# Kernel tuning notes

Hardware: AMD Instinct MI355X
Metric: run time of the kernel (lower is better)

Reference implementation:

```python
import jax, jax.numpy as jnp
import numpy as np

B, T, F, E = 256, 100, 34, 1024


def setup_inputs() -> dict:
    key = jax.random.key(0)
    ks = jax.random.split(key, 12)
    sc = 1.0 / np.sqrt(E)
    u = lambda k, shape: jax.random.uniform(k, shape, jnp.float32, -sc, sc)
    return {
        "x": jax.random.normal(ks[0], (B, T, F), jnp.float32),
        "W_lin": u(ks[1], (E, F)),
        "b_lin": u(ks[2], (E,)),
        "W_ih1": u(ks[3], (4 * E, E)),
        "W_hh1": u(ks[4], (4 * E, E)),
        "b_ih1": u(ks[5], (4 * E,)),
        "b_hh1": u(ks[6], (4 * E,)),
        "W_ih2": u(ks[7], (4 * E, E)),
        "W_hh2": u(ks[8], (4 * E, E)),
        "b_ih2": u(ks[9], (4 * E,)),
        "b_hh2": u(ks[10], (4 * E,)),
    }


def _gate_update(gates, c):
    # torch LSTMCell gate order: input, forget, cell(g), output
    i, f, g, o = jnp.split(gates, 4, axis=-1)
    c_new = jax.nn.sigmoid(f) * c + jax.nn.sigmoid(i) * jnp.tanh(g)
    h_new = jax.nn.sigmoid(o) * jnp.tanh(c_new)
    return h_new, c_new


def reference(x, W_lin, b_lin, W_ih1, W_hh1, b_ih1, b_hh1, W_ih2, W_hh2, b_ih2, b_hh2):
    hd = W_hh1.shape[1]
    bsz = x.shape[0]
    enc = x @ W_lin.T + b_lin                      # [B,T,E]
    # Precompute layer-1 input projections (incl. both biases) for all timesteps
    xg1 = jnp.einsum('bte,ge->btg', enc, W_ih1) + (b_ih1 + b_hh1)  # [B,T,4E]
    xs = jnp.swapaxes(xg1, 0, 1)                   # [T,B,4E] time-major for scan
    b2 = b_ih2 + b_hh2
    z = jnp.zeros((bsz, hd), jnp.float32)

    def step(carry, xg):
        h1, c1, h2, c2 = carry
        h1, c1 = _gate_update(xg + h1 @ W_hh1.T, c1)
        h2, c2 = _gate_update(h1 @ W_ih2.T + b2 + h2 @ W_hh2.T, c2)
        return (h1, c1, h2, c2), None

    (h1, c1, h2, c2), _ = jax.lax.scan(step, (z, z, z, z), xs)
    return (h2, c2)
```

## Files before the change

### kernel.cpp

```cpp
#include <hip/hip_runtime.h>

#define USH unsigned short
#define AGENT __HIP_MEMORY_SCOPE_AGENT
typedef __attribute__((ext_vector_type(8))) short short8;
typedef __attribute__((ext_vector_type(4))) float f32x4;

__device__ __forceinline__ USH rne_bf16(float f){
  unsigned int u = __float_as_uint(f);
  u = (u + 0x7fffu + ((u >> 16) & 1u)) >> 16;
  return (USH)u;
}
__device__ __forceinline__ float sigm(float x){ return 1.f / (1.f + __expf(-x)); }
__device__ __forceinline__ float tanh_(float x){ return 1.f - 2.f / (__expf(2.f * x) + 1.f); }
__device__ __forceinline__ void gload16(const void* g, void* l){
  __builtin_amdgcn_global_load_lds((const __attribute__((address_space(1))) unsigned int*)g,
                                   (__attribute__((address_space(3))) unsigned int*)l, 16, 0, 0);
}
__device__ __forceinline__ void st_bf16_sc1(USH* p, USH v){
  asm volatile("global_store_short %0, %1, off sc1" :: "v"(p), "v"((unsigned int)v) : "memory");
}
#define MFMA __builtin_amdgcn_mfma_f32_16x16x32_bf16

__global__ void k_fold(const float* __restrict__ Wih1, const float* __restrict__ Wlin,
                       const float* __restrict__ blin, const float* __restrict__ bih1,
                       const float* __restrict__ bhh1, USH* __restrict__ Wcpk, float* __restrict__ bc){
  const int n = blockIdx.x;
  const int t = threadIdx.x;
  float a[34];
#pragma unroll
  for (int f = 0; f < 34; ++f) a[f] = 0.f;
  float ab = 0.f;
  for (int e = t; e < 1024; e += 64){
    const float wv = Wih1[n * 1024 + e];
    ab += wv * blin[e];
    const float* wl = Wlin + e * 34;
#pragma unroll
    for (int f = 0; f < 34; ++f) a[f] += wv * wl[f];
  }
#pragma unroll
  for (int off = 32; off > 0; off >>= 1){
    ab += __shfl_down(ab, off);
#pragma unroll
    for (int f = 0; f < 34; ++f) a[f] += __shfl_down(a[f], off);
  }
  if (t == 0){
    const int nc = n & 1023, gq = n >> 10, cgi = nc >> 4, lp = nc & 15;
    for (int f = 0; f < 64; ++f){
      const float v = (f < 34) ? a[f] : 0.f;
      const int lane = lp + (((f >> 3) & 3) << 4);
      const int idx = (((cgi * 2 + (f >> 5)) * 4 + gq) * 64 + lane) * 8 + (f & 7);
      Wcpk[idx] = rne_bf16(v);
    }
    bc[n] = ab + bih1[n] + bhh1[n];
  }
}

__global__ void k_pack(const float* __restrict__ Whh1, const float* __restrict__ Wih2,
                       const float* __restrict__ Whh2, const float* __restrict__ bih2,
                       const float* __restrict__ bhh2,
                       USH* __restrict__ P1, USH* __restrict__ P2a, USH* __restrict__ P2b,
                       float* __restrict__ ob2){
  const int N = 4096 * 1024;
  for (int i = blockIdx.x * blockDim.x + threadIdx.x; i < N; i += gridDim.x * blockDim.x){
    const int j = i & 7, li = (i >> 3) & 63, gq = (i >> 9) & 3, ks = (i >> 11) & 31, cgi = i >> 16;
    const int n = gq * 1024 + cgi * 16 + (li & 15);
    const int k = ks * 32 + ((li >> 4) << 3) + j;
    const int src = n * 1024 + k;
    P1[i]  = rne_bf16(Whh1[src]);
    P2a[i] = rne_bf16(Wih2[src]);
    P2b[i] = rne_bf16(Whh2[src]);
    if (i < 4096) ob2[i] = bih2[i] + bhh2[i];
  }
}

__global__ void k_xpk(const float* __restrict__ x, USH* __restrict__ xp){
  const int N = 100 * 16384;
  for (int i = blockIdx.x * blockDim.x + threadIdx.x; i < N; i += gridDim.x * blockDim.x){
    const int j = i & 7, li = (i >> 3) & 63, ks = (i >> 9) & 1, g = (i >> 10) & 15, t = i >> 14;
    const int row = g * 16 + (li & 15);
    const int f = ks * 32 + ((li >> 4) << 3) + j;
    xp[i] = (f < 34) ? rne_bf16(x[(row * 100 + t) * 34 + f]) : (USH)0;
  }
}

__global__ __launch_bounds__(256) void k_persist(
    USH* __restrict__ hA1, USH* __restrict__ hA2,
    int* __restrict__ ctrA, int* __restrict__ ctrB,
    const USH* __restrict__ Wpk1, const USH* __restrict__ Wpk2a, const USH* __restrict__ Wpk2b,
    const USH* __restrict__ Wcpk, const USH* __restrict__ xpk,
    const float* __restrict__ bc, const float* __restrict__ b2, float* __restrict__ out,
    int d1, int d2, int useFence)
{
  __shared__ __attribute__((aligned(16))) char lds[131072];
  const int tid = threadIdx.x, w = tid >> 6, l = tid & 63;
  const int wg = blockIdx.x;
  const int isL2 = wg >> 7;
  const int cg = (wg & 127) >> 1;
  const int mh = wg & 1;
  const int gb = mh * 8 + w * 2;
  const int col = cg * 16 + (l & 15);
  const int lofs16 = l * 16;
  const int lofs8 = l * 8;

  if (!isL2){
    const USH* s = Wpk1 + (size_t)cg * 65536;
#pragma unroll
    for (int r = 0; r < 32; ++r)
      gload16(s + (r * 4 + w) * 512 + lofs8, &lds[(r * 4 + w) * 1024]);
  } else {
    const USH* s = Wpk2b + (size_t)cg * 65536;
#pragma unroll
    for (int r = 0; r < 24; ++r)
      gload16(s + (r * 4 + w) * 512 + lofs8, &lds[(r * 4 + w) * 1024]);
  }

  short8 wc[2][4];
  if (!isL2){
#pragma unroll
    for (int ks = 0; ks < 2; ++ks)
#pragma unroll
      for (int gq = 0; gq < 4; ++gq)
        wc[ks][gq] = *(const short8*)(Wcpk + (size_t)cg * 4096 + (ks * 4 + gq) * 512 + lofs8);
  }
  __syncthreads();

  float bi0, bi1, bi2, bi3;
  { const float* bs = isL2 ? b2 : bc;
    bi0 = bs[col]; bi1 = bs[1024 + col]; bi2 = bs[2048 + col]; bi3 = bs[3072 + col]; }

  float creg[2][4];
#pragma unroll
  for (int mf = 0; mf < 2; ++mf)
#pragma unroll
    for (int r = 0; r < 4; ++r) creg[mf][r] = 0.f;

  const int ks2 = cg >> 1;
  const int l16 = (cg * 2 + ((l & 15) >> 3)) & 3;
  const int j2 = l & 7;

  for (int p = 0; p <= 100; ++p){
    const bool active = isL2 ? (p >= 1) : (p < 100);
    if (active){
      f32x4 acc[2][4];
#pragma unroll
      for (int mf = 0; mf < 2; ++mf)
#pragma unroll
        for (int gq = 0; gq < 4; ++gq) acc[mf][gq] = (f32x4){0.f, 0.f, 0.f, 0.f};

      if (!isL2){
        if (p > 0){
          const USH* Ap = hA1 + (size_t)((p - 1) % d1) * 262144 + gb * 16384 + lofs8;
#pragma unroll
          for (int ks = 0; ks < 32; ++ks){
            short8 a0 = *(const short8*)(Ap + ks * 512);
            short8 a1 = *(const short8*)(Ap + 16384 + ks * 512);
            const char* bb = &lds[ks * 4096 + lofs16];
#pragma unroll
            for (int gq = 0; gq < 4; ++gq){
              short8 bf = *(const short8*)(bb + gq * 1024);
              acc[0][gq] = MFMA(a0, bf, acc[0][gq], 0, 0, 0);
              acc[1][gq] = MFMA(a1, bf, acc[1][gq], 0, 0, 0);
            }
          }
        }
        const USH* Xp = xpk + (size_t)p * 16384 + gb * 1024 + lofs8;
#pragma unroll
        for (int ks = 0; ks < 2; ++ks){
          short8 a0 = *(const short8*)(Xp + ks * 512);
          short8 a1 = *(const short8*)(Xp + 1024 + ks * 512);
#pragma unroll
          for (int gq = 0; gq < 4; ++gq){
            acc[0][gq] = MFMA(a0, wc[ks][gq], acc[0][gq], 0, 0, 0);
            acc[1][gq] = MFMA(a1, wc[ks][gq], acc[1][gq], 0, 0, 0);
          }
        }
        USH* hn = hA1 + (size_t)(p % d1) * 262144;
#pragma unroll
        for (int mf = 0; mf < 2; ++mf){
          const int g2 = gb + mf;
#pragma unroll
          for (int r = 0; r < 4; ++r){
            const float gi = acc[mf][0][r] + bi0;
            const float gf = acc[mf][1][r] + bi1;
            const float gg = acc[mf][2][r] + bi2;
            const float go = acc[mf][3][r] + bi3;
            const float cn = sigm(gf) * creg[mf][r] + sigm(gi) * tanh_(gg);
            creg[mf][r] = cn;
            const int lane2 = ((l >> 4) << 2) + r + (l16 << 4);
            st_bf16_sc1(&hn[(g2 * 32 + ks2) * 512 + lane2 * 8 + j2], rne_bf16(sigm(go) * tanh_(cn)));
          }
        }
      } else {
        const USH* A1p = hA1 + (size_t)((p - 1) % d1) * 262144 + gb * 16384 + lofs8;
        const USH* A2p = hA2 + (size_t)((p - 1) % d2) * 262144 + gb * 16384 + lofs8;
        const USH* Wsa = Wpk2a + (size_t)cg * 65536;
        const USH* Wsb = Wpk2b + (size_t)cg * 65536;
        short8 ar[2][8];
#pragma unroll
        for (int r = 0; r < 4; ++r)
          gload16(Wsa + (r * 4 + w) * 512 + lofs8, &lds[98304 + (r * 4 + w) * 1024]);
#pragma unroll
        for (int kk = 0; kk < 4; ++kk){
          ar[0][kk * 2]     = *(const short8*)(A1p + kk * 512);
          ar[0][kk * 2 + 1] = *(const short8*)(A1p + 16384 + kk * 512);
        }
#pragma unroll
        for (int c = 0; c < 10; ++c){
          __syncthreads();
          if (c < 9){
            const int t = c + 1;
            const USH* src = (t < 8) ? (Wsa + t * 8192) : (Wsb + (t - 2) * 8192);
            char* dst = &lds[98304 + (t & 1) * 16384];
#pragma unroll
            for (int r = 0; r < 4; ++r)
              gload16(src + (r * 4 + w) * 512 + lofs8, dst + (r * 4 + w) * 1024);
            const USH* Ab = (t < 8) ? A1p : A2p;
            const int ksb = (t < 8) ? t * 4 : (t - 2) * 4;
#pragma unroll
            for (int kk = 0; kk < 4; ++kk){
              ar[t & 1][kk * 2]     = *(const short8*)(Ab + (ksb + kk) * 512);
              ar[t & 1][kk * 2 + 1] = *(const short8*)(Ab + 16384 + (ksb + kk) * 512);
            }
          }
          const char* cb = &lds[98304 + (c & 1) * 16384 + lofs16];
#pragma unroll
          for (int kk = 0; kk < 4; ++kk){
#pragma unroll
            for (int gq = 0; gq < 4; ++gq){
              short8 bf = *(const short8*)(cb + kk * 4096 + gq * 1024);
              acc[0][gq] = MFMA(ar[c & 1][kk * 2],     bf, acc[0][gq], 0, 0, 0);
              acc[1][gq] = MFMA(ar[c & 1][kk * 2 + 1], bf, acc[1][gq], 0, 0, 0);
            }
          }
        }
#pragma unroll
        for (int ks = 0; ks < 24; ++ks){
          short8 a0 = *(const short8*)(A2p + ks * 512);
          short8 a1 = *(const short8*)(A2p + 16384 + ks * 512);
          const char* bb = &lds[ks * 4096 + lofs16];
#pragma unroll
          for (int gq = 0; gq < 4; ++gq){
            short8 bf = *(const short8*)(bb + gq * 1024);
            acc[0][gq] = MFMA(a0, bf, acc[0][gq], 0, 0, 0);
            acc[1][gq] = MFMA(a1, bf, acc[1][gq], 0, 0, 0);
          }
        }
        if (p < 100){
          USH* hn = hA2 + (size_t)(p % d2) * 262144;
#pragma unroll
          for (int mf = 0; mf < 2; ++mf){
            const int g2 = gb + mf;
#pragma unroll
            for (int r = 0; r < 4; ++r){
              const float gi = acc[mf][0][r] + bi0;
              const float gf = acc[mf][1][r] + bi1;
              const float gg = acc[mf][2][r] + bi2;
              const float go = acc[mf][3][r] + bi3;
              const float cn = sigm(gf) * creg[mf][r] + sigm(gi) * tanh_(gg);
              creg[mf][r] = cn;
              const int lane2 = ((l >> 4) << 2) + r + (l16 << 4);
              st_bf16_sc1(&hn[(g2 * 32 + ks2) * 512 + lane2 * 8 + j2], rne_bf16(sigm(go) * tanh_(cn)));
            }
          }
        } else {
#pragma unroll
          for (int mf = 0; mf < 2; ++mf){
#pragma unroll
            for (int r = 0; r < 4; ++r){
              const int row = (gb + mf) * 16 + ((l >> 4) << 2) + r;
              const float gi = acc[mf][0][r] + bi0;
              const float gf = acc[mf][1][r] + bi1;
              const float gg = acc[mf][2][r] + bi2;
              const float go = acc[mf][3][r] + bi3;
              const float cn = sigm(gf) * creg[mf][r] + sigm(gi) * tanh_(gg);
              out[row * 1024 + col] = sigm(go) * tanh_(cn);
              out[262144 + row * 1024 + col] = cn;
            }
          }
        }
      }
    }
    if (p < 100){
      asm volatile("s_waitcnt vmcnt(0)" ::: "memory");
      __syncthreads();
      if (tid == 0){
        if (useFence) __builtin_amdgcn_fence(__ATOMIC_RELEASE, "agent");
        __hip_atomic_fetch_add(isL2 ? ctrB : ctrA, 1, __ATOMIC_RELAXED, AGENT);
        const int q = p + 1;
        const int tA = 128 * q;
        const int tB = isL2 ? 128 * q : 128 * (q - 1);
        while (__hip_atomic_load(ctrA, __ATOMIC_RELAXED, AGENT) < tA)
          __builtin_amdgcn_s_sleep(1);
        while (__hip_atomic_load(ctrB, __ATOMIC_RELAXED, AGENT) < tB)
          __builtin_amdgcn_s_sleep(1);
        if (useFence) __builtin_amdgcn_fence(__ATOMIC_ACQUIRE, "agent");
      }
      __syncthreads();
    }
  }
}

extern "C" void kernel_launch(void* const* d_in, const int* in_sizes, int n_in,
                              void* d_out, int out_size, void* d_ws, size_t ws_size,
                              hipStream_t stream){
  const float* x    = (const float*)d_in[0];
  const float* Wlin = (const float*)d_in[1];
  const float* blin = (const float*)d_in[2];
  const float* Wih1 = (const float*)d_in[3];
  const float* Whh1 = (const float*)d_in[4];
  const float* bih1 = (const float*)d_in[5];
  const float* bhh1 = (const float*)d_in[6];
  const float* Wih2 = (const float*)d_in[7];
  const float* Whh2 = (const float*)d_in[8];
  const float* bih2 = (const float*)d_in[9];
  const float* bhh2 = (const float*)d_in[10];
  char* ws = (char*)d_ws;

  const size_t SLOT = 524288;
  int d1 = 100, d2 = 100, useFence = 0;
  const size_t need = 1024 + 200 * SLOT + 3 * 8388608ull + 524288 + 3276800 + 32768;
  if (ws_size < need){ d1 = 3; d2 = 2; useFence = 1; }

  size_t off = 0;
  int*   ctrA  = (int*)(ws + off);  off += 128;
  int*   ctrB  = (int*)(ws + off);  off = 1024;
  USH*   hA2   = (USH*)(ws + off);  off += (size_t)d2 * SLOT;
  USH*   hA1   = (USH*)(ws + off);  off += (size_t)d1 * SLOT;
  USH*   Wpk1  = (USH*)(ws + off);  off += 8388608;
  USH*   Wpk2a = (USH*)(ws + off);  off += 8388608;
  USH*   Wpk2b = (USH*)(ws + off);  off += 8388608;
  USH*   Wcpk  = (USH*)(ws + off);  off += 524288;
  USH*   xpk   = (USH*)(ws + off);  off += 3276800;
  float* bc    = (float*)(ws + off); off += 16384;
  float* b2    = (float*)(ws + off);

  hipMemsetAsync(ws, 0, 1024 + 2 * SLOT, stream);
  k_fold<<<4096, 64, 0, stream>>>(Wih1, Wlin, blin, bih1, bhh1, Wcpk, bc);
  k_pack<<<2048, 256, 0, stream>>>(Whh1, Wih2, Whh2, bih2, bhh2, Wpk1, Wpk2a, Wpk2b, b2);
  k_xpk<<<1024, 256, 0, stream>>>(x, xpk);

  float* outp = (float*)d_out;
  void* args[] = {&hA1, &hA2, &ctrA, &ctrB, &Wpk1, &Wpk2a, &Wpk2b, &Wcpk, &xpk, &bc, &b2, &outp,
                  &d1, &d2, &useFence};
  hipError_t e = hipLaunchCooperativeKernel((void*)k_persist, dim3(256), dim3(256), args, 0, stream);
  if (e != hipSuccess){
    k_persist<<<dim3(256), dim3(256), 0, stream>>>(hA1, hA2, ctrA, ctrB, Wpk1, Wpk2a, Wpk2b,
                                                   Wcpk, xpk, bc, b2, outp, d1, d2, useFence);
  }
}
```

Measured before the change: 1.760 ms.

## Split layer loops and relax grid barrier to per-layer dependency waits

```diff
diff --git a/kernel.cpp b/kernel.cpp
--- a/kernel.cpp
+++ b/kernel.cpp
@@ -102,79 +102,190 @@
   const int lofs16 = l * 16;
   const int lofs8 = l * 8;
 
-  if (!isL2){
-    const USH* s = Wpk1 + (size_t)cg * 65536;
-#pragma unroll
-    for (int r = 0; r < 32; ++r)
-      gload16(s + (r * 4 + w) * 512 + lofs8, &lds[(r * 4 + w) * 1024]);
-  } else {
-    const USH* s = Wpk2b + (size_t)cg * 65536;
-#pragma unroll
-    for (int r = 0; r < 24; ++r)
-      gload16(s + (r * 4 + w) * 512 + lofs8, &lds[(r * 4 + w) * 1024]);
-  }
-
-  short8 wc[2][4];
-  if (!isL2){
-#pragma unroll
-    for (int ks = 0; ks < 2; ++ks)
-#pragma unroll
-      for (int gq = 0; gq < 4; ++gq)
-        wc[ks][gq] = *(const short8*)(Wcpk + (size_t)cg * 4096 + (ks * 4 + gq) * 512 + lofs8);
-  }
-  __syncthreads();
-
-  float bi0, bi1, bi2, bi3;
-  { const float* bs = isL2 ? b2 : bc;
-    bi0 = bs[col]; bi1 = bs[1024 + col]; bi2 = bs[2048 + col]; bi3 = bs[3072 + col]; }
-
-  float creg[2][4];
-#pragma unroll
-  for (int mf = 0; mf < 2; ++mf)
-#pragma unroll
-    for (int r = 0; r < 4; ++r) creg[mf][r] = 0.f;
-
   const int ks2 = cg >> 1;
   const int l16 = (cg * 2 + ((l & 15) >> 3)) & 3;
   const int j2 = l & 7;
 
-  for (int p = 0; p <= 100; ++p){
-    const bool active = isL2 ? (p >= 1) : (p < 100);
-    if (active){
+  float creg[2][4];
+#pragma unroll
+  for (int mf = 0; mf < 2; ++mf)
+#pragma unroll
+    for (int r = 0; r < 4; ++r) creg[mf][r] = 0.f;
+
+  if (!isL2){
+    const USH* s = Wpk1 + (size_t)cg * 65536;
+#pragma unroll
+    for (int r = 0; r < 32; ++r)
+      gload16(s + (r * 4 + w) * 512 + lofs8, &lds[(r * 4 + w) * 1024]);
+    short8 wc[2][4];
+#pragma unroll
+    for (int ks = 0; ks < 2; ++ks)
+#pragma unroll
+      for (int gq = 0; gq < 4; ++gq)
+        wc[ks][gq] = *(const short8*)(Wcpk + (size_t)cg * 4096 + (ks * 4 + gq) * 512 + lofs8);
+    __syncthreads();
+    const float bi0 = bc[col], bi1 = bc[1024 + col], bi2 = bc[2048 + col], bi3 = bc[3072 + col];
+
+    for (int p = 0; p < 100; ++p){
+      if (p >= 1){
+        if (tid == 0){
+          while (__hip_atomic_load(ctrA, __ATOMIC_RELAXED, AGENT) < 128 * p)
+            __builtin_amdgcn_s_sleep(1);
+          if (useFence){
+            while (__hip_atomic_load(ctrB, __ATOMIC_RELAXED, AGENT) < 128 * (p - 2))
+              __builtin_amdgcn_s_sleep(1);
+            __builtin_amdgcn_fence(__ATOMIC_ACQUIRE, "agent");
+          }
+        }
+        __syncthreads();
+      }
       f32x4 acc[2][4];
 #pragma unroll
       for (int mf = 0; mf < 2; ++mf)
 #pragma unroll
         for (int gq = 0; gq < 4; ++gq) acc[mf][gq] = (f32x4){0.f, 0.f, 0.f, 0.f};
 
-      if (!isL2){
-        if (p > 0){
-          const USH* Ap = hA1 + (size_t)((p - 1) % d1) * 262144 + gb * 16384 + lofs8;
-#pragma unroll
-          for (int ks = 0; ks < 32; ++ks){
-            short8 a0 = *(const short8*)(Ap + ks * 512);
-            short8 a1 = *(const short8*)(Ap + 16384 + ks * 512);
-            const char* bb = &lds[ks * 4096 + lofs16];
+      if (p > 0){
+        const USH* Ap = hA1 + (size_t)((p - 1) % d1) * 262144 + gb * 16384 + lofs8;
+#pragma unroll
+        for (int ks = 0; ks < 32; ++ks){
+          short8 a0 = *(const short8*)(Ap + ks * 512);
+          short8 a1 = *(const short8*)(Ap + 16384 + ks * 512);
+          const char* bb = &lds[ks * 4096 + lofs16];
+#pragma unroll
+          for (int gq = 0; gq < 4; ++gq){
+            short8 bf = *(const short8*)(bb + gq * 1024);
+            acc[0][gq] = MFMA(a0, bf, acc[0][gq], 0, 0, 0);
+            acc[1][gq] = MFMA(a1, bf, acc[1][gq], 0, 0, 0);
+          }
+        }
+      }
+      const USH* Xp = xpk + (size_t)p * 16384 + gb * 1024 + lofs8;
+#pragma unroll
+      for (int ks = 0; ks < 2; ++ks){
+        short8 a0 = *(const short8*)(Xp + ks * 512);
+        short8 a1 = *(const short8*)(Xp + 1024 + ks * 512);
+#pragma unroll
+        for (int gq = 0; gq < 4; ++gq){
+          acc[0][gq] = MFMA(a0, wc[ks][gq], acc[0][gq], 0, 0, 0);
+          acc[1][gq] = MFMA(a1, wc[ks][gq], acc[1][gq], 0, 0, 0);
+        }
+      }
+      USH* hn = hA1 + (size_t)(p % d1) * 262144;
+#pragma unroll
+      for (int mf = 0; mf < 2; ++mf){
+        const int g2 = gb + mf;
+#pragma unroll
+        for (int r = 0; r < 4; ++r){
+          const float gi = acc[mf][0][r] + bi0;
+          const float gf = acc[mf][1][r] + bi1;
+          const float gg = acc[mf][2][r] + bi2;
+          const float go = acc[mf][3][r] + bi3;
+          const float cn = sigm(gf) * creg[mf][r] + sigm(gi) * tanh_(gg);
+          creg[mf][r] = cn;
+          const int lane2 = ((l >> 4) << 2) + r + (l16 << 4);
+          st_bf16_sc1(&hn[(g2 * 32 + ks2) * 512 + lane2 * 8 + j2], rne_bf16(sigm(go) * tanh_(cn)));
+        }
+      }
+      asm volatile("s_waitcnt vmcnt(0)" ::: "memory");
+      __syncthreads();
+      if (tid == 0){
+        if (useFence) __builtin_amdgcn_fence(__ATOMIC_RELEASE, "agent");
+        __hip_atomic_fetch_add(ctrA, 1, __ATOMIC_RELAXED, AGENT);
+      }
+    }
+  } else {
+    const USH* s = Wpk2b + (size_t)cg * 65536;
+#pragma unroll
+    for (int r = 0; r < 24; ++r)
+      gload16(s + (r * 4 + w) * 512 + lofs8, &lds[(r * 4 + w) * 1024]);
+    __syncthreads();
+    const float bi0 = b2[col], bi1 = b2[1024 + col], bi2 = b2[2048 + col], bi3 = b2[3072 + col];
+    const USH* Wsa = Wpk2a + (size_t)cg * 65536;
+    const USH* Wsb = Wpk2b + (size_t)cg * 65536;
+
+    for (int p = 1; p <= 100; ++p){
+#pragma unroll
+      for (int r = 0; r < 4; ++r)
+        gload16(Wsa + (r * 4 + w) * 512 + lofs8, &lds[98304 + (r * 4 + w) * 1024]);
+      if (tid == 0){
+        while (__hip_atomic_load(ctrA, __ATOMIC_RELAXED, AGENT) < 128 * p)
+          __builtin_amdgcn_s_sleep(1);
+        while (__hip_atomic_load(ctrB, __ATOMIC_RELAXED, AGENT) < 128 * (p - 1))
+          __builtin_amdgcn_s_sleep(1);
+        if (useFence) __builtin_amdgcn_fence(__ATOMIC_ACQUIRE, "agent");
+      }
+      __syncthreads();
+
+      const USH* A1p = hA1 + (size_t)((p - 1) % d1) * 262144 + gb * 16384 + lofs8;
+      const USH* A2p = hA2 + (size_t)((p - 1) % d2) * 262144 + gb * 16384 + lofs8;
+
+      f32x4 acc[2][4];
+#pragma unroll
+      for (int mf = 0; mf < 2; ++mf)
+#pragma unroll
+        for (int gq = 0; gq < 4; ++gq) acc[mf][gq] = (f32x4){0.f, 0.f, 0.f, 0.f};
+
+      short8 ar[2][8];
+#pragma unroll
+      for (int kk = 0; kk < 4; ++kk){
+        ar[0][kk * 2]     = *(const short8*)(A1p + kk * 512);
+        ar[0][kk * 2 + 1] = *(const short8*)(A1p + 16384 + kk * 512);
+      }
+#pragma unroll
+      for (int c = 0; c < 10; ++c){
+        if (c) __syncthreads();
+        if (c < 9){
+          const int t = c + 1;
+          const USH* src = (t < 8) ? (Wsa + t * 8192) : (Wsb + (t - 2) * 8192);
+          char* dst = &lds[98304 + (t & 1) * 16384];
+#pragma unroll
+          for (int r = 0; r < 4; ++r)
+            gload16(src + (r * 4 + w) * 512 + lofs8, dst + (r * 4 + w) * 1024);
+          const USH* Ab = (t < 8) ? A1p : A2p;
+          const int ksb = (t < 8) ? t * 4 : (t - 2) * 4;
+#pragma unroll
+          for (int kk = 0; kk < 4; ++kk){
+            ar[t & 1][kk * 2]     = *(const short8*)(Ab + (ksb + kk) * 512);
+            ar[t & 1][kk * 2 + 1] = *(const short8*)(Ab + 16384 + (ksb + kk) * 512);
+          }
+        }
+        const int rb = (c < 8) ? 2 * c : 16 + 4 * (c - 8);
+        const int rn = (c < 8) ? 2 : 4;
+        short8 ra[4][2];
+#pragma unroll
+        for (int q = 0; q < 4; ++q){
+          if (q < rn){
+            ra[q][0] = *(const short8*)(A2p + (rb + q) * 512);
+            ra[q][1] = *(const short8*)(A2p + 16384 + (rb + q) * 512);
+          }
+        }
+        const char* cb = &lds[98304 + (c & 1) * 16384 + lofs16];
+#pragma unroll
+        for (int kk = 0; kk < 4; ++kk){
+#pragma unroll
+          for (int gq = 0; gq < 4; ++gq){
+            short8 bf = *(const short8*)(cb + kk * 4096 + gq * 1024);
+            acc[0][gq] = MFMA(ar[c & 1][kk * 2],     bf, acc[0][gq], 0, 0, 0);
+            acc[1][gq] = MFMA(ar[c & 1][kk * 2 + 1], bf, acc[1][gq], 0, 0, 0);
+          }
+        }
+#pragma unroll
+        for (int q = 0; q < 4; ++q){
+          if (q < rn){
+            const char* bb = &lds[(rb + q) * 4096 + lofs16];
 #pragma unroll
             for (int gq = 0; gq < 4; ++gq){
               short8 bf = *(const short8*)(bb + gq * 1024);
-              acc[0][gq] = MFMA(a0, bf, acc[0][gq], 0, 0, 0);
-              acc[1][gq] = MFMA(a1, bf, acc[1][gq], 0, 0, 0);
+              acc[0][gq] = MFMA(ra[q][0], bf, acc[0][gq], 0, 0, 0);
+              acc[1][gq] = MFMA(ra[q][1], bf, acc[1][gq], 0, 0, 0);
             }
           }
         }
-        const USH* Xp = xpk + (size_t)p * 16384 + gb * 1024 + lofs8;
-#pragma unroll
-        for (int ks = 0; ks < 2; ++ks){
-          short8 a0 = *(const short8*)(Xp + ks * 512);
-          short8 a1 = *(const short8*)(Xp + 1024 + ks * 512);
-#pragma unroll
-          for (int gq = 0; gq < 4; ++gq){
-            acc[0][gq] = MFMA(a0, wc[ks][gq], acc[0][gq], 0, 0, 0);
-            acc[1][gq] = MFMA(a1, wc[ks][gq], acc[1][gq], 0, 0, 0);
-          }
-        }
-        USH* hn = hA1 + (size_t)(p % d1) * 262144;
+      }
+
+      if (p < 100){
+        USH* hn = hA2 + (size_t)(p % d2) * 262144;
 #pragma unroll
         for (int mf = 0; mf < 2; ++mf){
           const int g2 = gb + mf;
@@ -191,111 +302,27 @@
           }
         }
       } else {
-        const USH* A1p = hA1 + (size_t)((p - 1) % d1) * 262144 + gb * 16384 + lofs8;
-        const USH* A2p = hA2 + (size_t)((p - 1) % d2) * 262144 + gb * 16384 + lofs8;
-        const USH* Wsa = Wpk2a + (size_t)cg * 65536;
-        const USH* Wsb = Wpk2b + (size_t)cg * 65536;
-        short8 ar[2][8];
-#pragma unroll
-        for (int r = 0; r < 4; ++r)
-          gload16(Wsa + (r * 4 + w) * 512 + lofs8, &lds[98304 + (r * 4 + w) * 1024]);
-#pragma unroll
-        for (int kk = 0; kk < 4; ++kk){
-          ar[0][kk * 2]     = *(const short8*)(A1p + kk * 512);
-          ar[0][kk * 2 + 1] = *(const short8*)(A1p + 16384 + kk * 512);
-        }
-#pragma unroll
-        for (int c = 0; c < 10; ++c){
-          __syncthreads();
-          if (c < 9){
-            const int t = c + 1;
-            const USH* src = (t < 8) ? (Wsa + t * 8192) : (Wsb + (t - 2) * 8192);
-            char* dst = &lds[98304 + (t & 1) * 16384];
-#pragma unroll
-            for (int r = 0; r < 4; ++r)
-              gload16(src + (r * 4 + w) * 512 + lofs8, dst + (r * 4 + w) * 1024);
-            const USH* Ab = (t < 8) ? A1p : A2p;
-            const int ksb = (t < 8) ? t * 4 : (t - 2) * 4;
-#pragma unroll
-            for (int kk = 0; kk < 4; ++kk){
-              ar[t & 1][kk * 2]     = *(const short8*)(Ab + (ksb + kk) * 512);
-              ar[t & 1][kk * 2 + 1] = *(const short8*)(Ab + 16384 + (ksb + kk) * 512);
-            }
-          }
-          const char* cb = &lds[98304 + (c & 1) * 16384 + lofs16];
-#pragma unroll
-          for (int kk = 0; kk < 4; ++kk){
-#pragma unroll
-            for (int gq = 0; gq < 4; ++gq){
-              short8 bf = *(const short8*)(cb + kk * 4096 + gq * 1024);
-              acc[0][gq] = MFMA(ar[c & 1][kk * 2],     bf, acc[0][gq], 0, 0, 0);
-              acc[1][gq] = MFMA(ar[c & 1][kk * 2 + 1], bf, acc[1][gq], 0, 0, 0);
-            }
-          }
-        }
-#pragma unroll
-        for (int ks = 0; ks < 24; ++ks){
-          short8 a0 = *(const short8*)(A2p + ks * 512);
-          short8 a1 = *(const short8*)(A2p + 16384 + ks * 512);
-          const char* bb = &lds[ks * 4096 + lofs16];
-#pragma unroll
-          for (int gq = 0; gq < 4; ++gq){
-            short8 bf = *(const short8*)(bb + gq * 1024);
-            acc[0][gq] = MFMA(a0, bf, acc[0][gq], 0, 0, 0);
-            acc[1][gq] = MFMA(a1, bf, acc[1][gq], 0, 0, 0);
-          }
-        }
-        if (p < 100){
-          USH* hn = hA2 + (size_t)(p % d2) * 262144;
-#pragma unroll
-          for (int mf = 0; mf < 2; ++mf){
-            const int g2 = gb + mf;
-#pragma unroll
-            for (int r = 0; r < 4; ++r){
-              const float gi = acc[mf][0][r] + bi0;
-              const float gf = acc[mf][1][r] + bi1;
-              const float gg = acc[mf][2][r] + bi2;
-              const float go = acc[mf][3][r] + bi3;
-              const float cn = sigm(gf) * creg[mf][r] + sigm(gi) * tanh_(gg);
-              creg[mf][r] = cn;
-              const int lane2 = ((l >> 4) << 2) + r + (l16 << 4);
-              st_bf16_sc1(&hn[(g2 * 32 + ks2) * 512 + lane2 * 8 + j2], rne_bf16(sigm(go) * tanh_(cn)));
-            }
-          }
-        } else {
-#pragma unroll
-          for (int mf = 0; mf < 2; ++mf){
-#pragma unroll
-            for (int r = 0; r < 4; ++r){
-              const int row = (gb + mf) * 16 + ((l >> 4) << 2) + r;
-              const float gi = acc[mf][0][r] + bi0;
-              const float gf = acc[mf][1][r] + bi1;
-              const float gg = acc[mf][2][r] + bi2;
-              const float go = acc[mf][3][r] + bi3;
-              const float cn = sigm(gf) * creg[mf][r] + sigm(gi) * tanh_(gg);
-              out[row * 1024 + col] = sigm(go) * tanh_(cn);
-              out[262144 + row * 1024 + col] = cn;
-            }
-          }
-        }
-      }
-    }
-    if (p < 100){
+#pragma unroll
+        for (int mf = 0; mf < 2; ++mf){
+#pragma unroll
+          for (int r = 0; r < 4; ++r){
+            const int row = (gb + mf) * 16 + ((l >> 4) << 2) + r;
+            const float gi = acc[mf][0][r] + bi0;
+            const float gf = acc[mf][1][r] + bi1;
+            const float gg = acc[mf][2][r] + bi2;
+            const float go = acc[mf][3][r] + bi3;
+            const float cn = sigm(gf) * creg[mf][r] + sigm(gi) * tanh_(gg);
+            out[row * 1024 + col] = sigm(go) * tanh_(cn);
+            out[262144 + row * 1024 + col] = cn;
+          }
+        }
+      }
       asm volatile("s_waitcnt vmcnt(0)" ::: "memory");
       __syncthreads();
       if (tid == 0){
         if (useFence) __builtin_amdgcn_fence(__ATOMIC_RELEASE, "agent");
-        __hip_atomic_fetch_add(isL2 ? ctrB : ctrA, 1, __ATOMIC_RELAXED, AGENT);
-        const int q = p + 1;
-        const int tA = 128 * q;
-        const int tB = isL2 ? 128 * q : 128 * (q - 1);
-        while (__hip_atomic_load(ctrA, __ATOMIC_RELAXED, AGENT) < tA)
-          __builtin_amdgcn_s_sleep(1);
-        while (__hip_atomic_load(ctrB, __ATOMIC_RELAXED, AGENT) < tB)
-          __builtin_amdgcn_s_sleep(1);
-        if (useFence) __builtin_amdgcn_fence(__ATOMIC_ACQUIRE, "agent");
-      }
-      __syncthreads();
+        __hip_atomic_fetch_add(ctrB, 1, __ATOMIC_RELAXED, AGENT);
+      }
     }
   }
 }
@@ -334,7 +361,7 @@
   float* bc    = (float*)(ws + off); off += 16384;
   float* b2    = (float*)(ws + off);
 
-  hipMemsetAsync(ws, 0, 1024 + 2 * SLOT, stream);
+  hipMemsetAsync(ws, 0, 1024 + SLOT, stream);
   k_fold<<<4096, 64, 0, stream>>>(Wih1, Wlin, blin, bih1, bhh1, Wcpk, bc);
   k_pack<<<2048, 256, 0, stream>>>(Whh1, Wih2, Whh2, bih2, bhh2, Wpk1, Wpk2a, Wpk2b, b2);
   k_xpk<<<1024, 256, 0, stream>>>(x, xpk);
```

Measured after the change: 1.823 ms. 1.04x slower.
